# Optimization experiments

Hardware: AMD Instinct MI355X
Metric: run time of the kernel (lower is better)

The kernel has to match this reference:

```python
import jax, jax.numpy as jnp
import numpy as np

B, C, N, H = 4, 256, 2048, 8
D = C // 4  # q/k projection dim
BN_EPS = 1e-5


def setup_inputs() -> dict:
    key = jax.random.key(0)
    ks = jax.random.split(key, 16)
    s = lambda fan: 1.0 / np.sqrt(fan)
    return {
        "x": jax.random.normal(ks[0], (B, C, N), dtype=jnp.float32),
        # per-head params, stacked on leading head axis
        "w_qk": jax.random.normal(ks[1], (H, D, C), dtype=jnp.float32) * s(C),  # shared q/k conv weight
        "w_v": jax.random.normal(ks[2], (H, C, C), dtype=jnp.float32) * s(C),
        "b_v": jax.random.normal(ks[3], (H, C), dtype=jnp.float32) * 0.01,
        "w_t": jax.random.normal(ks[4], (H, C, C), dtype=jnp.float32) * s(C),
        "b_t": jax.random.normal(ks[5], (H, C), dtype=jnp.float32) * 0.01,
        "bn_g": jnp.ones((H, C), dtype=jnp.float32),
        "bn_b": jnp.zeros((H, C), dtype=jnp.float32),
        "bn_m": jax.random.normal(ks[6], (H, C), dtype=jnp.float32) * 0.1,
        "bn_v": jax.random.uniform(ks[7], (H, C), dtype=jnp.float32, minval=0.5, maxval=1.5),
        # final 1x1 conv + BN (LeakyReLU 0.2)
        "w_lin": jax.random.normal(ks[8], (C, C * H), dtype=jnp.float32) * s(C * H),
        "lbn_g": jnp.ones((C,), dtype=jnp.float32),
        "lbn_b": jnp.zeros((C,), dtype=jnp.float32),
        "lbn_m": jax.random.normal(ks[9], (C,), dtype=jnp.float32) * 0.1,
        "lbn_v": jax.random.uniform(ks[10], (C,), dtype=jnp.float32, minval=0.5, maxval=1.5),
    }


def _oa_head(x, w_qk, w_v, b_v, w_t, b_t, g, b, m, v):
    # x: [B, C, N]; 1x1 Conv1d == channel matmul
    x_q = jnp.einsum("dc,bcn->bnd", w_qk, x)                 # [B, N, D]
    x_k = jnp.einsum("dc,bcn->bdn", w_qk, x)                 # [B, D, N] (shared weight)
    x_v = jnp.einsum("ec,bcn->ben", w_v, x) + b_v[:, None]   # [B, C, N]
    energy = jnp.einsum("bnd,bdm->bnm", x_q, x_k)            # [B, N, N]
    attn = jax.nn.softmax(energy, axis=-1)
    attn = attn / (1e-9 + attn.sum(axis=1, keepdims=True))   # extra L1 renorm over dim=1
    x_r = jnp.einsum("ben,bnm->bem", x_v, attn)              # [B, C, N]
    y = jnp.einsum("ec,bcn->ben", w_t, x - x_r) + b_t[:, None]
    y = (y - m[:, None]) * (g[:, None] / jnp.sqrt(v[:, None] + BN_EPS)) + b[:, None]
    return x + jax.nn.relu(y)


def reference(x, w_qk, w_v, b_v, w_t, b_t, bn_g, bn_b, bn_m, bn_v,
              w_lin, lbn_g, lbn_b, lbn_m, lbn_v):
    # run all H heads via vmap over stacked params -> [B, H, C, N]
    heads = jax.vmap(_oa_head, in_axes=(None, 0, 0, 0, 0, 0, 0, 0, 0, 0), out_axes=1)(
        x, w_qk, w_v, b_v, w_t, b_t, bn_g, bn_b, bn_m, bn_v)
    cat = heads.reshape(x.shape[0], H * C, x.shape[2])       # torch.cat(dim=1) order
    y = jnp.einsum("ck,bkn->bcn", w_lin, cat)                # 1x1 conv, no bias
    y = (y - lbn_m[:, None]) * (lbn_g[:, None] / jnp.sqrt(lbn_v[:, None] + BN_EPS)) + lbn_b[:, None]
    return jnp.where(y >= 0, y, 0.2 * y)                     # LeakyReLU(0.2)
```

## Files before the change

### kernel.cpp

```cpp
#include <hip/hip_runtime.h>
#include <math.h>

#define B_ 4
#define C_ 256
#define N_ 2048
#define H_ 8
#define D_ 64
#define BH_ 32
#define HC_ 2048
#define BN_EPS 1e-5f
#define SCL 1.2011224087864498f

typedef __attribute__((ext_vector_type(8))) short s8v;
typedef __attribute__((ext_vector_type(4))) short s4v;
typedef __attribute__((ext_vector_type(8))) _Float16 h8v;
typedef __attribute__((ext_vector_type(4))) float f32x4;

#define MFMA __builtin_amdgcn_mfma_f32_16x16x32_bf16
#define MFMAH __builtin_amdgcn_mfma_f32_16x16x32_f16

static __device__ __forceinline__ unsigned short f2b(float f) {
  union { float f; unsigned int i; } v; v.f = f;
  unsigned int r = v.i + 0x7FFFu + ((v.i >> 16) & 1u);
  return (unsigned short)(r >> 16);
}
static __device__ __forceinline__ float b2f(unsigned short u) {
  union { unsigned int i; float f; } v; v.i = ((unsigned int)u) << 16;
  return v.f;
}
static __device__ __forceinline__ float fexp2(float x) {
  float r;
  asm("v_exp_f32 %0, %1" : "=v"(r) : "v"(x));
  return r;
}
static __device__ __forceinline__ unsigned cvtpk(float lo, float hi) {
  unsigned r;
  asm("v_cvt_pk_bf16_f32 %0, %1, %2" : "=v"(r) : "v"(lo), "v"(hi));
  return r;
}
static __device__ __forceinline__ void gload16(const void* g, void* l) {
  __builtin_amdgcn_global_load_lds(
      (const __attribute__((address_space(1))) unsigned int*)g,
      (__attribute__((address_space(3))) unsigned int*)l, 16, 0, 0);
}

struct GP {
  const float *x, *w_qk, *w_v, *b_v, *w_t, *b_t, *bn_g, *bn_b, *bn_m, *bn_v;
  const float *w_lin, *lbn_g, *lbn_b, *lbn_m, *lbn_v;
  _Float16 *PT;
  short *xThi, *xTlo, *HOT, *wvb, *wtb, *wlinb, *wqkh, *wqkl, *Vb, *xmr;
  float *part, *shb, *nrm, *sh, *out;
};

__global__ __launch_bounds__(256) void cvt_k(const float* __restrict__ in,
                                             short* __restrict__ out) {
  int i = (blockIdx.x * 256 + threadIdx.x) * 4;
  float4 v = *(const float4*)(in + i);
  s4v o = { (short)f2b(v.x), (short)f2b(v.y), (short)f2b(v.z), (short)f2b(v.w) };
  *(s4v*)(out + i) = o;
}

__global__ __launch_bounds__(256) void cvtqk_k(const float* __restrict__ in,
                                               short* __restrict__ oh,
                                               short* __restrict__ ol) {
  int i = (blockIdx.x * 256 + threadIdx.x) * 4;
  float4 v = *(const float4*)(in + i);
  float a[4] = {v.x, v.y, v.z, v.w};
  s4v h, l;
#pragma unroll
  for (int e = 0; e < 4; ++e) {
    unsigned short hu = f2b(a[e]);
    h[e] = (short)hu;
    l[e] = (short)f2b(a[e] - b2f(hu));
  }
  *(s4v*)(oh + i) = h;
  *(s4v*)(ol + i) = l;
}

__global__ __launch_bounds__(256) void xsplit_k(const float* __restrict__ x,
                                                short* __restrict__ xh,
                                                short* __restrict__ xl) {
  const int n0 = blockIdx.x * 64, c0 = blockIdx.y * 64, b = blockIdx.z;
  const float* xb = x + (size_t)b * C_ * N_;
  __shared__ float sm[64][65];
  const int t = threadIdx.x;
#pragma unroll
  for (int i = 0; i < 4; ++i) {
    int idx = i * 256 + t;
    int c = idx >> 4, j = (idx & 15) * 4;
    float4 v = *(const float4*)(xb + (size_t)(c0 + c) * N_ + n0 + j);
    sm[j + 0][c] = v.x; sm[j + 1][c] = v.y; sm[j + 2][c] = v.z; sm[j + 3][c] = v.w;
  }
  __syncthreads();
#pragma unroll
  for (int i = 0; i < 2; ++i) {
    int idx = i * 256 + t;
    int n = idx >> 3, cg = (idx & 7) * 8;
    s8v hh, ll;
#pragma unroll
    for (int d = 0; d < 8; ++d) {
      float v = sm[n][cg + d];
      unsigned short hu = f2b(v);
      hh[d] = (short)hu;
      ll[d] = (short)f2b(v - b2f(hu));
    }
    size_t o = ((size_t)b * N_ + n0 + n) * C_ + c0 + cg;
    *(s8v*)(xh + o) = hh;
    *(s8v*)(xl + o) = ll;
  }
}

__global__ __launch_bounds__(256, 2) void p_k(GP p) {
  const int t = threadIdx.x, wv = t >> 6, lane = t & 63;
  const int l15 = lane & 15, l4 = lane >> 4;
  const int n0 = blockIdx.x * 128;
  const int bh = blockIdx.y, b = bh / H_, h = bh % H_;
  const short* Ah_g = p.wqkh + h * D_ * C_;
  const short* Al_g = p.wqkl + h * D_ * C_;
  const short* Bh_g = p.xThi + (size_t)b * N_ * C_;
  const short* Bl_g = p.xTlo + (size_t)b * N_ * C_;
  __shared__ short AsH[64 * 64], AsL[64 * 64], BsH[128 * 64], BsL[128 * 64];
  __shared__ float Tr[128 * 65];
  f32x4 acc[4][2] = {};
  for (int kc = 0; kc < 256; kc += 64) {
    __syncthreads();
#pragma unroll
    for (int i = 0; i < 2; ++i) {
      int idx = i * 256 + t;
      int row = idx >> 3, offl = (idx & 7) * 16;
      int so = offl ^ ((row & 7) << 4);
      gload16((const char*)(Ah_g + (size_t)row * C_ + kc) + so, (char*)AsH + idx * 16);
      gload16((const char*)(Al_g + (size_t)row * C_ + kc) + so, (char*)AsL + idx * 16);
    }
#pragma unroll
    for (int i = 0; i < 4; ++i) {
      int idx = i * 256 + t;
      int row = idx >> 3, offl = (idx & 7) * 16;
      int so = offl ^ ((row & 7) << 4);
      gload16((const char*)(Bh_g + (size_t)(n0 + row) * C_ + kc) + so, (char*)BsH + idx * 16);
      gload16((const char*)(Bl_g + (size_t)(n0 + row) * C_ + kc) + so, (char*)BsL + idx * 16);
    }
    __syncthreads();
    s8v adh[4][2], adl[4][2], bnh[2][2], bnl[2][2];
#pragma unroll
    for (int d = 0; d < 4; ++d)
#pragma unroll
      for (int ks = 0; ks < 2; ++ks) {
        int row = d * 16 + l15;
        int byte = row * 128 + ((ks * 64 + l4 * 16) ^ ((row & 7) << 4));
        adh[d][ks] = *(const s8v*)((const char*)AsH + byte);
        adl[d][ks] = *(const s8v*)((const char*)AsL + byte);
      }
#pragma unroll
    for (int nb = 0; nb < 2; ++nb)
#pragma unroll
      for (int ks = 0; ks < 2; ++ks) {
        int row = wv * 32 + nb * 16 + l15;
        int byte = row * 128 + ((ks * 64 + l4 * 16) ^ ((row & 7) << 4));
        bnh[nb][ks] = *(const s8v*)((const char*)BsH + byte);
        bnl[nb][ks] = *(const s8v*)((const char*)BsL + byte);
      }
#pragma unroll
    for (int d = 0; d < 4; ++d)
#pragma unroll
      for (int nb = 0; nb < 2; ++nb) {
        acc[d][nb] = MFMA(adh[d][0], bnh[nb][0], acc[d][nb], 0, 0, 0);
        acc[d][nb] = MFMA(adh[d][1], bnh[nb][1], acc[d][nb], 0, 0, 0);
        acc[d][nb] = MFMA(adh[d][0], bnl[nb][0], acc[d][nb], 0, 0, 0);
        acc[d][nb] = MFMA(adh[d][1], bnl[nb][1], acc[d][nb], 0, 0, 0);
        acc[d][nb] = MFMA(adl[d][0], bnh[nb][0], acc[d][nb], 0, 0, 0);
        acc[d][nb] = MFMA(adl[d][1], bnh[nb][1], acc[d][nb], 0, 0, 0);
      }
  }
  __syncthreads();
#pragma unroll
  for (int d = 0; d < 4; ++d)
#pragma unroll
    for (int nb = 0; nb < 2; ++nb)
#pragma unroll
      for (int r = 0; r < 4; ++r) {
        int n_l = wv * 32 + nb * 16 + l15;
        int dd = d * 16 + l4 * 4 + r;
        Tr[n_l * 65 + dd] = acc[d][nb][r];
      }
  __syncthreads();
  _Float16* Pf = p.PT + ((size_t)bh * N_ + n0) * D_;
  float* nz = p.nrm + (size_t)bh * N_;
#pragma unroll
  for (int i = 0; i < 4; ++i) {
    int idx = i * 256 + t;
    int n = idx >> 3, dg = (idx & 7) * 8;
    h8v hv;
    float ssq = 0.f;
#pragma unroll
    for (int j = 0; j < 8; ++j) {
      float v = Tr[n * 65 + dg + j] * SCL;
      ssq = fmaf(v, v, ssq);
      hv[j] = (_Float16)v;
    }
    *(h8v*)(Pf + (size_t)n * D_ + dg) = hv;
    ssq += __shfl_xor(ssq, 1, 64);
    ssq += __shfl_xor(ssq, 2, 64);
    ssq += __shfl_xor(ssq, 4, 64);
    if ((t & 7) == 0) nz[n0 + n] = ssq;
  }
}

__global__ __launch_bounds__(256) void shift_k(const float* __restrict__ nrm,
                                               float* __restrict__ sh) {
  const int z = blockIdx.x, t = threadIdx.x;
  const float* nz = nrm + (size_t)z * N_;
  float loc[8];
  float mx = 0.f;
#pragma unroll
  for (int i = 0; i < 8; ++i) {
    loc[i] = nz[i * 256 + t];
    mx = fmaxf(mx, loc[i]);
  }
  for (int o = 32; o; o >>= 1) mx = fmaxf(mx, __shfl_xor(mx, o, 64));
  __shared__ float sb[4];
  if ((t & 63) == 0) sb[t >> 6] = mx;
  __syncthreads();
  float M = sqrtf(fmaxf(fmaxf(sb[0], sb[1]), fmaxf(sb[2], sb[3])));
#pragma unroll
  for (int i = 0; i < 8; ++i)
    sh[(size_t)z * N_ + i * 256 + t] = sqrtf(loc[i]) * M;
}

__global__ __launch_bounds__(256, 4) void passa_k(GP p) {
  const int t = threadIdx.x, wv = t >> 6, lane = t & 63;
  const int l15 = lane & 15, l4 = lane >> 4;
  const int wr = wv >> 1, wc = wv & 1;
  const int z = blockIdx.x;
  int idx = blockIdx.y;
  int ti = 0;
  while (idx >= 16 - ti) { idx -= 16 - ti; ++ti; }
  const int tj = ti + idx;
  const int r0 = ti * 128, c0 = tj * 128;
  const _Float16* Pz = p.PT + (size_t)z * N_ * D_;
  const float* shz = p.sh + (size_t)z * N_;
  __shared__ short RH[8192], CH[8192];
  __shared__ float rbuf[2][2][64], cbuf[2][2][64];
#pragma unroll
  for (int i = 0; i < 4; ++i) {
    int c2 = i * 256 + t;
    int row = c2 >> 3, offl = (c2 & 7) * 16;
    int so = offl ^ ((row & 7) << 4);
    gload16((const char*)(Pz + (size_t)(r0 + row) * D_) + so, (char*)RH + c2 * 16);
    if (ti != tj)
      gload16((const char*)(Pz + (size_t)(c0 + row) * D_) + so, (char*)CH + c2 * 16);
  }
  __syncthreads();
  const char* BHp = (ti == tj) ? (const char*)RH : (const char*)CH;

  h8v bh4[4][2];
  float shc[4];
#pragma unroll
  for (int nf = 0; nf < 4; ++nf) {
#pragma unroll
    for (int ks = 0; ks < 2; ++ks) {
      int row = wc * 64 + nf * 16 + l15;
      int byte = row * 128 + ((ks * 64 + l4 * 16) ^ ((row & 7) << 4));
      bh4[nf][ks] = *(const h8v*)(BHp + byte);
    }
    shc[nf] = shz[c0 + wc * 64 + nf * 16 + l15];
  }
  float rowp[4][4] = {};
  float colp[4] = {};
#pragma unroll
  for (int mf = 0; mf < 4; ++mf) {
    h8v ah[2];
#pragma unroll
    for (int ks = 0; ks < 2; ++ks) {
      int row = wr * 64 + mf * 16 + l15;
      int byte = row * 128 + ((ks * 64 + l4 * 16) ^ ((row & 7) << 4));
      ah[ks] = *(const h8v*)((const char*)RH + byte);
    }
    f32x4 shr = *(const f32x4*)(shz + r0 + wr * 64 + mf * 16 + l4 * 4);
#pragma unroll
    for (int nf = 0; nf < 4; ++nf) {
      f32x4 s = {};
      s = MFMAH(ah[0], bh4[nf][0], s, 0, 0, 0);
      s = MFMAH(ah[1], bh4[nf][1], s, 0, 0, 0);
      rowp[mf][0] += fexp2(s[0] - shr[0]);
      rowp[mf][1] += fexp2(s[1] - shr[1]);
      rowp[mf][2] += fexp2(s[2] - shr[2]);
      rowp[mf][3] += fexp2(s[3] - shr[3]);
      if (ti != tj)
        colp[nf] += fexp2(s[0] - shc[nf]) + fexp2(s[1] - shc[nf]) +
                    fexp2(s[2] - shc[nf]) + fexp2(s[3] - shc[nf]);
    }
  }
#pragma unroll
  for (int mf = 0; mf < 4; ++mf)
#pragma unroll
    for (int r = 0; r < 4; ++r) {
      float v = rowp[mf][r];
      v += __shfl_xor(v, 1, 64); v += __shfl_xor(v, 2, 64);
      v += __shfl_xor(v, 4, 64); v += __shfl_xor(v, 8, 64);
      rowp[mf][r] = v;
    }
#pragma unroll
  for (int nf = 0; nf < 4; ++nf) {
    float v = colp[nf];
    v += __shfl_xor(v, 16, 64); v += __shfl_xor(v, 32, 64);
    colp[nf] = v;
  }
  if (l15 == 0)
#pragma unroll
    for (int mf = 0; mf < 4; ++mf)
#pragma unroll
      for (int r = 0; r < 4; ++r)
        rbuf[wr][wc][mf * 16 + l4 * 4 + r] = rowp[mf][r];
  if (l4 == 0)
#pragma unroll
    for (int nf = 0; nf < 4; ++nf)
      cbuf[wc][wr][nf * 16 + l15] = colp[nf];
  __syncthreads();
  if (t < 128) {
    float v = rbuf[t >> 6][0][t & 63] + rbuf[t >> 6][1][t & 63];
    p.part[((size_t)z * 16 + tj) * N_ + r0 + t] = v;
  } else if (ti != tj) {
    int u = t - 128;
    float v = cbuf[u >> 6][0][u & 63] + cbuf[u >> 6][1][u & 63];
    p.part[((size_t)z * 16 + ti) * N_ + c0 + u] = v;
  }
}

__global__ __launch_bounds__(256) void shbred_k(const float* __restrict__ part,
                                                const float* __restrict__ sh,
                                                float* __restrict__ shb) {
  int i = blockIdx.x * 256 + threadIdx.x;
  int z = i >> 11, n = i & 2047;
  const float* pz = part + ((size_t)z * 16) * N_ + n;
  float s = 0.f;
#pragma unroll
  for (int j = 0; j < 16; ++j) s += pz[(size_t)j * N_];
  shb[i] = sh[i] + __log2f(s);
}

__global__ __launch_bounds__(256, 2) void passb_k(GP p) {
  const int t = threadIdx.x, wv = t >> 6, lane = t & 63;
  const int l15 = lane & 15, l4 = lane >> 4;
  const int z = blockIdx.x, b = z / H_;
  const int m0 = blockIdx.y * 128;
  const _Float16* Pz = p.PT + (size_t)z * N_ * D_;
  const short* Vz = p.Vb + (size_t)z * C_ * N_;
  const float* shbz = p.shb + (size_t)z * N_;

  __shared__ char smem[57856];
  float* cs_sm = (float*)(smem + 49152);
  float* shs = (float*)(smem + 49664);

  h8v bm[2][2];
#pragma unroll
  for (int mf = 0; mf < 2; ++mf)
#pragma unroll
    for (int ks = 0; ks < 2; ++ks)
      bm[mf][ks] = *(const h8v*)(Pz + (size_t)(m0 + wv * 32 + mf * 16 + l15) * D_ + ks * 32 + l4 * 8);

  s8v va[4][2];

#define STAGE_PN(n0v, bufbyte) do { \
    _Pragma("unroll") \
    for (int i_ = 0; i_ < 2; ++i_) { \
      int sl_ = i_ * 256 + t; \
      int rw_ = sl_ >> 3, of_ = (sl_ & 7) * 16; \
      gload16((const char*)(Pz + (size_t)((n0v) + rw_) * D_) + (of_ ^ ((rw_ & 7) << 4)), \
              smem + (bufbyte) + sl_ * 16); \
    } \
  } while (0)
#define ISSUE_V(n0v) do { \
    _Pragma("unroll") \
    for (int eb = 0; eb < 4; ++eb) { \
      const short* vr_ = Vz + (size_t)(wv * 64 + eb * 16 + l15) * N_ + (n0v) + l4 * 8; \
      va[eb][0] = *(const s8v*)vr_; \
      va[eb][1] = *(const s8v*)(vr_ + 32); \
    } \
  } while (0)

  f32x4 racc[4][8] = {};
  float csa0 = 0.f, csa1 = 0.f;

  STAGE_PN(0, 0);
  STAGE_PN(64, 8192);
  ISSUE_V(0);
#pragma unroll
  for (int i = 0; i < 2; ++i) {
    int ii = i * 256 + t;
    *(float4*)(shs + ii * 4) = *(const float4*)(shbz + ii * 4);
  }
  __syncthreads();

  for (int it = 0; it < 32; ++it) {
    const int n0 = it * 64;
    const int cur = it & 1;
    const char* PH = smem + cur * 8192;
    char* AT = smem + 16384 + cur * 16384;
#pragma unroll
    for (int nb = 0; nb < 4; ++nb) {
      int rowb = nb * 16 + l15;
      int sw = (rowb & 7) << 4;
      h8v an0 = *(const h8v*)(PH + rowb * 128 + ((l4 * 16) ^ sw));
      h8v an1 = *(const h8v*)(PH + rowb * 128 + ((64 + l4 * 16) ^ sw));
      f32x4 s0 = {}, s1 = {};
      s0 = MFMAH(an0, bm[0][0], s0, 0, 0, 0);
      s0 = MFMAH(an1, bm[0][1], s0, 0, 0, 0);
      s1 = MFMAH(an0, bm[1][0], s1, 0, 0, 0);
      s1 = MFMAH(an1, bm[1][1], s1, 0, 0, 0);
      f32x4 sb4 = *(const f32x4*)(shs + n0 + nb * 16 + l4 * 4);
      float a0 = fexp2(s0[0] - sb4[0]);
      float a1 = fexp2(s0[1] - sb4[1]);
      float a2 = fexp2(s0[2] - sb4[2]);
      float a3 = fexp2(s0[3] - sb4[3]);
      float c0 = fexp2(s1[0] - sb4[0]);
      float c1 = fexp2(s1[1] - sb4[1]);
      float c2 = fexp2(s1[2] - sb4[2]);
      float c3 = fexp2(s1[3] - sb4[3]);
      csa0 += (a0 + a1) + (a2 + a3);
      csa1 += (c0 + c1) + (c2 + c3);
      uint2 pk0 = { cvtpk(a0, a1), cvtpk(a2, a3) };
      uint2 pk1 = { cvtpk(c0, c1), cvtpk(c2, c3) };
      int swm = (l15 & 7) << 4;
      int cb = (nb * 32 + l4 * 8);
      *(uint2*)(AT + (wv * 32 + l15) * 128 + (cb ^ swm)) = pk0;
      *(uint2*)(AT + (wv * 32 + 16 + l15) * 128 + (cb ^ swm)) = pk1;
    }
    asm volatile("s_waitcnt vmcnt(8) lgkmcnt(0)" ::: "memory");
    __builtin_amdgcn_s_barrier();
    __builtin_amdgcn_sched_barrier(0);
    if (it < 30) STAGE_PN(n0 + 128, cur * 8192);
    __builtin_amdgcn_s_setprio(1);
#pragma unroll
    for (int mb = 0; mb < 8; ++mb) {
      int rowb = mb * 16 + l15;
      int sw = (rowb & 7) << 4;
      s8v at0 = *(const s8v*)(AT + rowb * 128 + ((l4 * 16) ^ sw));
      s8v at1 = *(const s8v*)(AT + rowb * 128 + ((64 + l4 * 16) ^ sw));
#pragma unroll
      for (int eb = 0; eb < 4; ++eb) {
        racc[eb][mb] = MFMA(va[eb][0], at0, racc[eb][mb], 0, 0, 0);
        racc[eb][mb] = MFMA(va[eb][1], at1, racc[eb][mb], 0, 0, 0);
      }
    }
    __builtin_amdgcn_s_setprio(0);
    if (it < 31) ISSUE_V(n0 + 64);
  }

  csa0 += __shfl_xor(csa0, 16, 64);
  csa0 += __shfl_xor(csa0, 32, 64);
  csa1 += __shfl_xor(csa1, 16, 64);
  csa1 += __shfl_xor(csa1, 32, 64);
  if (l4 == 0) {
    cs_sm[wv * 32 + l15] = csa0;
    cs_sm[wv * 32 + 16 + l15] = csa1;
  }
  __syncthreads();
  float invc[8];
#pragma unroll
  for (int mb = 0; mb < 8; ++mb) invc[mb] = 1.0f / (1e-9f + cs_sm[mb * 16 + l15]);
  const float* xb = p.x + (size_t)b * C_ * N_;
  char* Tr = smem;
#pragma unroll
  for (int half = 0; half < 2; ++half) {
    if (half) __syncthreads();
#pragma unroll
    for (int eb = 0; eb < 4; ++eb)
#pragma unroll
      for (int mbh = 0; mbh < 4; ++mbh) {
        int mb = half * 4 + mbh;
        int e0 = wv * 64 + eb * 16 + l4 * 4;
        int m_l = mbh * 16 + l15;
        int mg = m0 + mb * 16 + l15;
        float v0 = xb[(size_t)(e0 + 0) * N_ + mg] - racc[eb][mb][0] * invc[mb];
        float v1 = xb[(size_t)(e0 + 1) * N_ + mg] - racc[eb][mb][1] * invc[mb];
        float v2 = xb[(size_t)(e0 + 2) * N_ + mg] - racc[eb][mb][2] * invc[mb];
        float v3 = xb[(size_t)(e0 + 3) * N_ + mg] - racc[eb][mb][3] * invc[mb];
        uint2 pk = { cvtpk(v0, v1), cvtpk(v2, v3) };
        *(uint2*)(Tr + m_l * 512 + ((e0 * 2) ^ ((m_l & 7) << 4))) = pk;
      }
    __syncthreads();
    short* xz = p.xmr + ((size_t)z * N_ + m0 + half * 64) * C_;
#pragma unroll
    for (int i = 0; i < 8; ++i) {
      int idx = i * 256 + t;
      int m_l = idx >> 5, off2 = (idx & 31) * 16;
      s8v v = *(const s8v*)(Tr + m_l * 512 + (off2 ^ ((m_l & 7) << 4)));
      *(s8v*)((char*)(xz + (size_t)m_l * C_) + off2) = v;
    }
  }
#undef STAGE_PN
#undef ISSUE_V
}

template<int EPI>
__global__ __launch_bounds__(256) void mm_k(GP p) {
  constexpr int K = (EPI == 4) ? 2048 : 256;
  const int t = threadIdx.x;
  const int wave = t >> 6, lane = t & 63;
  const int wr = wave >> 1, wc = wave & 1;
  const int l15 = lane & 15, l4 = lane >> 4;
  const int n0 = blockIdx.x * 128;
  const int m0 = blockIdx.y * 128;
  const int z = blockIdx.z;
  int bh = z, b = bh / H_, h = bh % H_;

  const short *Ag, *Bg;
  if constexpr (EPI == 1)      { Ag = p.wvb + h * C_ * C_; Bg = p.xThi + (size_t)b * N_ * C_; }
  else if constexpr (EPI == 3) { Ag = p.wtb + h * C_ * C_; Bg = p.xmr + (size_t)z * N_ * C_; }
  else                         { Ag = p.wlinb; Bg = p.HOT + (size_t)z * N_ * HC_; b = z; }

  __shared__ short As[128 * 32];
  __shared__ short Bs[128 * 32];

  f32x4 acc[4][4] = {};

  for (int k0 = 0; k0 < K; k0 += 32) {
    __syncthreads();
#pragma unroll
    for (int i = 0; i < 2; ++i) {
      int idx = i * 256 + t;
      int row = idx >> 2, kg = (idx & 3) * 8;
      gload16(Ag + (size_t)(m0 + row) * K + k0 + kg, (char*)As + idx * 16);
      gload16(Bg + (size_t)(n0 + row) * K + k0 + kg, (char*)Bs + idx * 16);
    }
    __syncthreads();
    s8v af[4], bf[4];
#pragma unroll
    for (int m = 0; m < 4; ++m) af[m] = *(const s8v*)&As[(wr * 64 + m * 16 + l15) * 32 + l4 * 8];
#pragma unroll
    for (int n = 0; n < 4; ++n) bf[n] = *(const s8v*)&Bs[(wc * 64 + n * 16 + l15) * 32 + l4 * 8];
#pragma unroll
    for (int m = 0; m < 4; ++m)
#pragma unroll
      for (int n = 0; n < 4; ++n)
        acc[m][n] = MFMA(af[m], bf[n], acc[m][n], 0, 0, 0);
  }

  if constexpr (EPI == 1) {
    short* Vz = p.Vb + (size_t)z * C_ * N_;
#pragma unroll
    for (int m = 0; m < 4; ++m)
#pragma unroll
      for (int r = 0; r < 4; ++r) {
        int e = m0 + wr * 64 + m * 16 + l4 * 4 + r;
        float bias = p.b_v[h * C_ + e];
#pragma unroll
        for (int n = 0; n < 4; ++n) {
          int c = n0 + wc * 64 + n * 16 + l15;
          Vz[(size_t)e * N_ + c] = (short)f2b(acc[m][n][r] + bias);
        }
      }
  } else if constexpr (EPI == 3) {
    __shared__ short Tr[128 * 128];
    const float* xb = p.x + (size_t)b * C_ * N_;
#pragma unroll
    for (int m = 0; m < 4; ++m)
#pragma unroll
      for (int r = 0; r < 4; ++r) {
        int e = m0 + wr * 64 + m * 16 + l4 * 4 + r;
        int el = e - m0;
        int hc = h * C_ + e;
        float bt = p.b_t[hc], mm = p.bn_m[hc], bb = p.bn_b[hc];
        float sc = p.bn_g[hc] / sqrtf(p.bn_v[hc] + BN_EPS);
#pragma unroll
        for (int n = 0; n < 4; ++n) {
          int cl = wc * 64 + n * 16 + l15;
          float y = (acc[m][n][r] + bt - mm) * sc + bb;
          float val = xb[(size_t)e * N_ + n0 + cl] + fmaxf(y, 0.f);
          Tr[cl * 128 + el] = (short)f2b(val);
        }
      }
    __syncthreads();
    short* Hz = p.HOT + (size_t)b * N_ * HC_;
#pragma unroll
    for (int it = 0; it < 8; ++it) {
      int idx = it * 256 + t;
      int cl = idx >> 4, eg = (idx & 15) * 8;
      *(s8v*)(Hz + (size_t)(n0 + cl) * HC_ + h * C_ + m0 + eg) = *(const s8v*)&Tr[cl * 128 + eg];
    }
  } else {
    float* ob = p.out + (size_t)b * C_ * N_;
#pragma unroll
    for (int m = 0; m < 4; ++m)
#pragma unroll
      for (int r = 0; r < 4; ++r) {
        int e = m0 + wr * 64 + m * 16 + l4 * 4 + r;
        float mm = p.lbn_m[e], bb = p.lbn_b[e];
        float sc = p.lbn_g[e] / sqrtf(p.lbn_v[e] + BN_EPS);
#pragma unroll
        for (int n = 0; n < 4; ++n) {
          int c = n0 + wc * 64 + n * 16 + l15;
          float y = (acc[m][n][r] - mm) * sc + bb;
          ob[(size_t)e * N_ + c] = y >= 0.f ? y : 0.2f * y;
        }
      }
  }
}

extern "C" void kernel_launch(void* const* d_in, const int* in_sizes, int n_in,
                              void* d_out, int out_size, void* d_ws, size_t ws_size,
                              hipStream_t stream) {
  GP p;
  p.x     = (const float*)d_in[0];
  p.w_qk  = (const float*)d_in[1];
  p.w_v   = (const float*)d_in[2];
  p.b_v   = (const float*)d_in[3];
  p.w_t   = (const float*)d_in[4];
  p.b_t   = (const float*)d_in[5];
  p.bn_g  = (const float*)d_in[6];
  p.bn_b  = (const float*)d_in[7];
  p.bn_m  = (const float*)d_in[8];
  p.bn_v  = (const float*)d_in[9];
  p.w_lin = (const float*)d_in[10];
  p.lbn_g = (const float*)d_in[11];
  p.lbn_b = (const float*)d_in[12];
  p.lbn_m = (const float*)d_in[13];
  p.lbn_v = (const float*)d_in[14];
  p.out   = (float*)d_out;

  char* base = (char*)d_ws;
  size_t off = 0;
  auto alloc = [&](size_t bytes) -> char* {
    char* r = base + off;
    off += (bytes + 255) & ~(size_t)255;
    return r;
  };
  p.PT    = (_Float16*)alloc((size_t)BH_ * N_ * D_ * 2);
  p.xThi  = (short*)alloc((size_t)B_ * N_ * C_ * 2);
  p.xTlo  = (short*)alloc((size_t)B_ * N_ * C_ * 2);
  p.wqkh  = (short*)alloc((size_t)H_ * D_ * C_ * 2);
  p.wqkl  = (short*)alloc((size_t)H_ * D_ * C_ * 2);
  p.wvb   = (short*)alloc((size_t)H_ * C_ * C_ * 2);
  p.wtb   = (short*)alloc((size_t)H_ * C_ * C_ * 2);
  p.wlinb = (short*)alloc((size_t)C_ * HC_ * 2);
  p.Vb    = (short*)alloc((size_t)BH_ * C_ * N_ * 2);
  p.xmr   = (short*)alloc((size_t)BH_ * N_ * C_ * 2);
  p.part  = (float*)alloc((size_t)BH_ * 16 * N_ * 4);
  p.shb   = (float*)alloc((size_t)BH_ * N_ * 4);
  p.nrm   = (float*)alloc((size_t)BH_ * N_ * 4);
  p.sh    = (float*)alloc((size_t)BH_ * N_ * 4);
  p.HOT   = p.Vb;

  dim3 blk(256);

  cvt_k<<<512, blk, 0, stream>>>(p.w_v, p.wvb);
  cvt_k<<<512, blk, 0, stream>>>(p.w_t, p.wtb);
  cvt_k<<<512, blk, 0, stream>>>(p.w_lin, p.wlinb);
  cvtqk_k<<<128, blk, 0, stream>>>(p.w_qk, p.wqkh, p.wqkl);
  xsplit_k<<<dim3(32, 4, B_), blk, 0, stream>>>(p.x, p.xThi, p.xTlo);
  p_k<<<dim3(16, BH_), blk, 0, stream>>>(p);
  shift_k<<<BH_, blk, 0, stream>>>(p.nrm, p.sh);
  mm_k<1><<<dim3(16, 2, BH_), blk, 0, stream>>>(p);
  passa_k<<<dim3(32, 136), blk, 0, stream>>>(p);
  shbred_k<<<256, blk, 0, stream>>>(p.part, p.sh, p.shb);
  passb_k<<<dim3(32, 16), blk, 0, stream>>>(p);
  mm_k<3><<<dim3(16, 2, BH_), blk, 0, stream>>>(p);
  mm_k<4><<<dim3(16, 2, B_), blk, 0, stream>>>(p);
}
```

Before: 248.0 us.

## Use single fp16 for QK/V projections and split final linear into smaller-tile kernel

Replaces the split hi/lo bf16 emulation of fp32 in the Q/K projection with a single fp16 pass, cutting its MFMA count and LDS/global traffic by a factor of three. The V projection now also uses fp16 inputs, which removes the separate xThi/xTlo buffers. The final 2048-deep linear layer moves to a dedicated kernel with 64x128 tiles and a 64-wide K step, which raises the block count from 128 to 256 for better CU occupancy. The risk is lower precision in the energy logits, since fp16 has fewer mantissa bits than split bf16 and those logits feed an exponential.

```diff
diff --git a/kernel.cpp b/kernel.cpp
--- a/kernel.cpp
+++ b/kernel.cpp
@@ -14,6 +14,7 @@
 typedef __attribute__((ext_vector_type(8))) short s8v;
 typedef __attribute__((ext_vector_type(4))) short s4v;
 typedef __attribute__((ext_vector_type(8))) _Float16 h8v;
+typedef __attribute__((ext_vector_type(4))) _Float16 h4v;
 typedef __attribute__((ext_vector_type(4))) float f32x4;
 
 #define MFMA __builtin_amdgcn_mfma_f32_16x16x32_bf16
@@ -24,10 +25,6 @@
   unsigned int r = v.i + 0x7FFFu + ((v.i >> 16) & 1u);
   return (unsigned short)(r >> 16);
 }
-static __device__ __forceinline__ float b2f(unsigned short u) {
-  union { unsigned int i; float f; } v; v.i = ((unsigned int)u) << 16;
-  return v.f;
-}
 static __device__ __forceinline__ float fexp2(float x) {
   float r;
   asm("v_exp_f32 %0, %1" : "=v"(r) : "v"(x));
@@ -47,8 +44,8 @@
 struct GP {
   const float *x, *w_qk, *w_v, *b_v, *w_t, *b_t, *bn_g, *bn_b, *bn_m, *bn_v;
   const float *w_lin, *lbn_g, *lbn_b, *lbn_m, *lbn_v;
-  _Float16 *PT;
-  short *xThi, *xTlo, *HOT, *wvb, *wtb, *wlinb, *wqkh, *wqkl, *Vb, *xmr;
+  _Float16 *PT, *xT, *wqk16, *wvh;
+  short *HOT, *wtb, *wlinb, *Vb, *xmr;
   float *part, *shb, *nrm, *sh, *out;
 };
 
@@ -60,26 +57,16 @@
   *(s4v*)(out + i) = o;
 }
 
-__global__ __launch_bounds__(256) void cvtqk_k(const float* __restrict__ in,
-                                               short* __restrict__ oh,
-                                               short* __restrict__ ol) {
+__global__ __launch_bounds__(256) void cvth_k(const float* __restrict__ in,
+                                              _Float16* __restrict__ out) {
   int i = (blockIdx.x * 256 + threadIdx.x) * 4;
   float4 v = *(const float4*)(in + i);
-  float a[4] = {v.x, v.y, v.z, v.w};
-  s4v h, l;
-#pragma unroll
-  for (int e = 0; e < 4; ++e) {
-    unsigned short hu = f2b(a[e]);
-    h[e] = (short)hu;
-    l[e] = (short)f2b(a[e] - b2f(hu));
-  }
-  *(s4v*)(oh + i) = h;
-  *(s4v*)(ol + i) = l;
-}
-
-__global__ __launch_bounds__(256) void xsplit_k(const float* __restrict__ x,
-                                                short* __restrict__ xh,
-                                                short* __restrict__ xl) {
+  h4v o = { (_Float16)v.x, (_Float16)v.y, (_Float16)v.z, (_Float16)v.w };
+  *(h4v*)(out + i) = o;
+}
+
+__global__ __launch_bounds__(256) void xcvt_k(const float* __restrict__ x,
+                                              _Float16* __restrict__ xT) {
   const int n0 = blockIdx.x * 64, c0 = blockIdx.y * 64, b = blockIdx.z;
   const float* xb = x + (size_t)b * C_ * N_;
   __shared__ float sm[64][65];
@@ -96,17 +83,10 @@
   for (int i = 0; i < 2; ++i) {
     int idx = i * 256 + t;
     int n = idx >> 3, cg = (idx & 7) * 8;
-    s8v hh, ll;
-#pragma unroll
-    for (int d = 0; d < 8; ++d) {
-      float v = sm[n][cg + d];
-      unsigned short hu = f2b(v);
-      hh[d] = (short)hu;
-      ll[d] = (short)f2b(v - b2f(hu));
-    }
-    size_t o = ((size_t)b * N_ + n0 + n) * C_ + c0 + cg;
-    *(s8v*)(xh + o) = hh;
-    *(s8v*)(xl + o) = ll;
+    h8v o;
+#pragma unroll
+    for (int d = 0; d < 8; ++d) o[d] = (_Float16)sm[n][cg + d];
+    *(h8v*)(xT + ((size_t)b * N_ + n0 + n) * C_ + c0 + cg) = o;
   }
 }
 
@@ -115,11 +95,9 @@
   const int l15 = lane & 15, l4 = lane >> 4;
   const int n0 = blockIdx.x * 128;
   const int bh = blockIdx.y, b = bh / H_, h = bh % H_;
-  const short* Ah_g = p.wqkh + h * D_ * C_;
-  const short* Al_g = p.wqkl + h * D_ * C_;
-  const short* Bh_g = p.xThi + (size_t)b * N_ * C_;
-  const short* Bl_g = p.xTlo + (size_t)b * N_ * C_;
-  __shared__ short AsH[64 * 64], AsL[64 * 64], BsH[128 * 64], BsL[128 * 64];
+  const _Float16* Ag = p.wqk16 + h * D_ * C_;
+  const _Float16* Bg = p.xT + (size_t)b * N_ * C_;
+  __shared__ _Float16 As[64 * 64], Bs[128 * 64];
   __shared__ float Tr[128 * 65];
   f32x4 acc[4][2] = {};
   for (int kc = 0; kc < 256; kc += 64) {
@@ -128,48 +106,38 @@
     for (int i = 0; i < 2; ++i) {
       int idx = i * 256 + t;
       int row = idx >> 3, offl = (idx & 7) * 16;
-      int so = offl ^ ((row & 7) << 4);
-      gload16((const char*)(Ah_g + (size_t)row * C_ + kc) + so, (char*)AsH + idx * 16);
-      gload16((const char*)(Al_g + (size_t)row * C_ + kc) + so, (char*)AsL + idx * 16);
+      gload16((const char*)(Ag + (size_t)row * C_ + kc) + (offl ^ ((row & 7) << 4)),
+              (char*)As + idx * 16);
     }
 #pragma unroll
     for (int i = 0; i < 4; ++i) {
       int idx = i * 256 + t;
       int row = idx >> 3, offl = (idx & 7) * 16;
-      int so = offl ^ ((row & 7) << 4);
-      gload16((const char*)(Bh_g + (size_t)(n0 + row) * C_ + kc) + so, (char*)BsH + idx * 16);
-      gload16((const char*)(Bl_g + (size_t)(n0 + row) * C_ + kc) + so, (char*)BsL + idx * 16);
-    }
-    __syncthreads();
-    s8v adh[4][2], adl[4][2], bnh[2][2], bnl[2][2];
+      gload16((const char*)(Bg + (size_t)(n0 + row) * C_ + kc) + (offl ^ ((row & 7) << 4)),
+              (char*)Bs + idx * 16);
+    }
+    __syncthreads();
+    h8v ad[4][2], bn[2][2];
 #pragma unroll
     for (int d = 0; d < 4; ++d)
 #pragma unroll
       for (int ks = 0; ks < 2; ++ks) {
         int row = d * 16 + l15;
-        int byte = row * 128 + ((ks * 64 + l4 * 16) ^ ((row & 7) << 4));
-        adh[d][ks] = *(const s8v*)((const char*)AsH + byte);
-        adl[d][ks] = *(const s8v*)((const char*)AsL + byte);
+        ad[d][ks] = *(const h8v*)((const char*)As + row * 128 + ((ks * 64 + l4 * 16) ^ ((row & 7) << 4)));
       }
 #pragma unroll
     for (int nb = 0; nb < 2; ++nb)
 #pragma unroll
       for (int ks = 0; ks < 2; ++ks) {
         int row = wv * 32 + nb * 16 + l15;
-        int byte = row * 128 + ((ks * 64 + l4 * 16) ^ ((row & 7) << 4));
-        bnh[nb][ks] = *(const s8v*)((const char*)BsH + byte);
-        bnl[nb][ks] = *(const s8v*)((const char*)BsL + byte);
+        bn[nb][ks] = *(const h8v*)((const char*)Bs + row * 128 + ((ks * 64 + l4 * 16) ^ ((row & 7) << 4)));
       }
 #pragma unroll
     for (int d = 0; d < 4; ++d)
 #pragma unroll
       for (int nb = 0; nb < 2; ++nb) {
-        acc[d][nb] = MFMA(adh[d][0], bnh[nb][0], acc[d][nb], 0, 0, 0);
-        acc[d][nb] = MFMA(adh[d][1], bnh[nb][1], acc[d][nb], 0, 0, 0);
-        acc[d][nb] = MFMA(adh[d][0], bnl[nb][0], acc[d][nb], 0, 0, 0);
-        acc[d][nb] = MFMA(adh[d][1], bnl[nb][1], acc[d][nb], 0, 0, 0);
-        acc[d][nb] = MFMA(adl[d][0], bnh[nb][0], acc[d][nb], 0, 0, 0);
-        acc[d][nb] = MFMA(adl[d][1], bnh[nb][1], acc[d][nb], 0, 0, 0);
+        acc[d][nb] = MFMAH(ad[d][0], bn[nb][0], acc[d][nb], 0, 0, 0);
+        acc[d][nb] = MFMAH(ad[d][1], bn[nb][1], acc[d][nb], 0, 0, 0);
       }
   }
   __syncthreads();
@@ -495,7 +463,7 @@
 
 template<int EPI>
 __global__ __launch_bounds__(256) void mm_k(GP p) {
-  constexpr int K = (EPI == 4) ? 2048 : 256;
+  constexpr int K = 256;
   const int t = threadIdx.x;
   const int wave = t >> 6, lane = t & 63;
   const int wr = wave >> 1, wc = wave & 1;
@@ -503,12 +471,16 @@
   const int n0 = blockIdx.x * 128;
   const int m0 = blockIdx.y * 128;
   const int z = blockIdx.z;
-  int bh = z, b = bh / H_, h = bh % H_;
+  int b = z / H_, h = z % H_;
 
   const short *Ag, *Bg;
-  if constexpr (EPI == 1)      { Ag = p.wvb + h * C_ * C_; Bg = p.xThi + (size_t)b * N_ * C_; }
-  else if constexpr (EPI == 3) { Ag = p.wtb + h * C_ * C_; Bg = p.xmr + (size_t)z * N_ * C_; }
-  else                         { Ag = p.wlinb; Bg = p.HOT + (size_t)z * N_ * HC_; b = z; }
+  if constexpr (EPI == 1) {
+    Ag = (const short*)(p.wvh + (size_t)h * C_ * C_);
+    Bg = (const short*)(p.xT + (size_t)b * N_ * C_);
+  } else {
+    Ag = p.wtb + (size_t)h * C_ * C_;
+    Bg = p.xmr + (size_t)z * N_ * C_;
+  }
 
   __shared__ short As[128 * 32];
   __shared__ short Bs[128 * 32];
@@ -533,8 +505,13 @@
 #pragma unroll
     for (int m = 0; m < 4; ++m)
 #pragma unroll
-      for (int n = 0; n < 4; ++n)
-        acc[m][n] = MFMA(af[m], bf[n], acc[m][n], 0, 0, 0);
+      for (int n = 0; n < 4; ++n) {
+        if constexpr (EPI == 1)
+          acc[m][n] = MFMAH(__builtin_bit_cast(h8v, af[m]), __builtin_bit_cast(h8v, bf[n]),
+                            acc[m][n], 0, 0, 0);
+        else
+          acc[m][n] = MFMA(af[m], bf[n], acc[m][n], 0, 0, 0);
+      }
   }
 
   if constexpr (EPI == 1) {
@@ -551,7 +528,7 @@
           Vz[(size_t)e * N_ + c] = (short)f2b(acc[m][n][r] + bias);
         }
       }
-  } else if constexpr (EPI == 3) {
+  } else {
     __shared__ short Tr[128 * 128];
     const float* xb = p.x + (size_t)b * C_ * N_;
 #pragma unroll
@@ -579,23 +556,74 @@
       int cl = idx >> 4, eg = (idx & 15) * 8;
       *(s8v*)(Hz + (size_t)(n0 + cl) * HC_ + h * C_ + m0 + eg) = *(const s8v*)&Tr[cl * 128 + eg];
     }
-  } else {
-    float* ob = p.out + (size_t)b * C_ * N_;
+  }
+}
+
+__global__ __launch_bounds__(256, 2) void mm4_k(GP p) {
+  const int t = threadIdx.x, wv = t >> 6, lane = t & 63;
+  const int l15 = lane & 15, l4 = lane >> 4;
+  const int n0 = blockIdx.x * 128;
+  const int m0 = blockIdx.y * 64;
+  const int b = blockIdx.z;
+  const short* Ag = p.wlinb;
+  const short* Bg = p.HOT + (size_t)b * N_ * HC_;
+  __shared__ short As[64 * 64], Bs[128 * 64];
+  f32x4 acc[4][2] = {};
+  for (int k0 = 0; k0 < HC_; k0 += 64) {
+    __syncthreads();
+#pragma unroll
+    for (int i = 0; i < 2; ++i) {
+      int sl = i * 256 + t;
+      int rw = sl >> 3, of = (sl & 7) * 16;
+      gload16((const char*)(Ag + (size_t)(m0 + rw) * HC_ + k0) + (of ^ ((rw & 7) << 4)),
+              (char*)As + sl * 16);
+    }
+#pragma unroll
+    for (int i = 0; i < 4; ++i) {
+      int sl = i * 256 + t;
+      int rw = sl >> 3, of = (sl & 7) * 16;
+      gload16((const char*)(Bg + (size_t)(n0 + rw) * HC_ + k0) + (of ^ ((rw & 7) << 4)),
+              (char*)Bs + sl * 16);
+    }
+    __syncthreads();
+    s8v af[4][2], bf[2][2];
 #pragma unroll
     for (int m = 0; m < 4; ++m)
 #pragma unroll
-      for (int r = 0; r < 4; ++r) {
-        int e = m0 + wr * 64 + m * 16 + l4 * 4 + r;
-        float mm = p.lbn_m[e], bb = p.lbn_b[e];
-        float sc = p.lbn_g[e] / sqrtf(p.lbn_v[e] + BN_EPS);
-#pragma unroll
-        for (int n = 0; n < 4; ++n) {
-          int c = n0 + wc * 64 + n * 16 + l15;
-          float y = (acc[m][n][r] - mm) * sc + bb;
-          ob[(size_t)e * N_ + c] = y >= 0.f ? y : 0.2f * y;
-        }
-      }
-  }
+      for (int ks = 0; ks < 2; ++ks) {
+        int rw = m * 16 + l15;
+        af[m][ks] = *(const s8v*)((const char*)As + rw * 128 + ((ks * 64 + l4 * 16) ^ ((rw & 7) << 4)));
+      }
+#pragma unroll
+    for (int nf = 0; nf < 2; ++nf)
+#pragma unroll
+      for (int ks = 0; ks < 2; ++ks) {
+        int rw = wv * 32 + nf * 16 + l15;
+        bf[nf][ks] = *(const s8v*)((const char*)Bs + rw * 128 + ((ks * 64 + l4 * 16) ^ ((rw & 7) << 4)));
+      }
+#pragma unroll
+    for (int m = 0; m < 4; ++m)
+#pragma unroll
+      for (int nf = 0; nf < 2; ++nf) {
+        acc[m][nf] = MFMA(af[m][0], bf[nf][0], acc[m][nf], 0, 0, 0);
+        acc[m][nf] = MFMA(af[m][1], bf[nf][1], acc[m][nf], 0, 0, 0);
+      }
+  }
+  float* ob = p.out + (size_t)b * C_ * N_;
+#pragma unroll
+  for (int m = 0; m < 4; ++m)
+#pragma unroll
+    for (int r = 0; r < 4; ++r) {
+      int e = m0 + m * 16 + l4 * 4 + r;
+      float mm = p.lbn_m[e], bb = p.lbn_b[e];
+      float sc = p.lbn_g[e] / sqrtf(p.lbn_v[e] + BN_EPS);
+#pragma unroll
+      for (int nf = 0; nf < 2; ++nf) {
+        int c = n0 + wv * 32 + nf * 16 + l15;
+        float y = (acc[m][nf][r] - mm) * sc + bb;
+        ob[(size_t)e * N_ + c] = y >= 0.f ? y : 0.2f * y;
+      }
+    }
 }
 
 extern "C" void kernel_launch(void* const* d_in, const int* in_sizes, int n_in,
@@ -627,11 +655,9 @@
     return r;
   };
   p.PT    = (_Float16*)alloc((size_t)BH_ * N_ * D_ * 2);
-  p.xThi  = (short*)alloc((size_t)B_ * N_ * C_ * 2);
-  p.xTlo  = (short*)alloc((size_t)B_ * N_ * C_ * 2);
-  p.wqkh  = (short*)alloc((size_t)H_ * D_ * C_ * 2);
-  p.wqkl  = (short*)alloc((size_t)H_ * D_ * C_ * 2);
-  p.wvb   = (short*)alloc((size_t)H_ * C_ * C_ * 2);
+  p.xT    = (_Float16*)alloc((size_t)B_ * N_ * C_ * 2);
+  p.wqk16 = (_Float16*)alloc((size_t)H_ * D_ * C_ * 2);
+  p.wvh   = (_Float16*)alloc((size_t)H_ * C_ * C_ * 2);
   p.wtb   = (short*)alloc((size_t)H_ * C_ * C_ * 2);
   p.wlinb = (short*)alloc((size_t)C_ * HC_ * 2);
   p.Vb    = (short*)alloc((size_t)BH_ * C_ * N_ * 2);
@@ -644,11 +670,11 @@
 
   dim3 blk(256);
 
-  cvt_k<<<512, blk, 0, stream>>>(p.w_v, p.wvb);
   cvt_k<<<512, blk, 0, stream>>>(p.w_t, p.wtb);
   cvt_k<<<512, blk, 0, stream>>>(p.w_lin, p.wlinb);
-  cvtqk_k<<<128, blk, 0, stream>>>(p.w_qk, p.wqkh, p.wqkl);
-  xsplit_k<<<dim3(32, 4, B_), blk, 0, stream>>>(p.x, p.xThi, p.xTlo);
+  cvth_k<<<128, blk, 0, stream>>>(p.w_qk, p.wqk16);
+  cvth_k<<<512, blk, 0, stream>>>(p.w_v, p.wvh);
+  xcvt_k<<<dim3(32, 4, B_), blk, 0, stream>>>(p.x, p.xT);
   p_k<<<dim3(16, BH_), blk, 0, stream>>>(p);
   shift_k<<<BH_, blk, 0, stream>>>(p.nrm, p.sh);
   mm_k<1><<<dim3(16, 2, BH_), blk, 0, stream>>>(p);
@@ -656,5 +682,5 @@
   shbred_k<<<256, blk, 0, stream>>>(p.part, p.sh, p.shb);
   passb_k<<<dim3(32, 16), blk, 0, stream>>>(p);
   mm_k<3><<<dim3(16, 2, BH_), blk, 0, stream>>>(p);
-  mm_k<4><<<dim3(16, 2, B_), blk, 0, stream>>>(p);
-}
+  mm4_k<<<dim3(16, 4, B_), blk, 0, stream>>>(p);
+}
```

Result: faster. 228.8 us (-7.8%).
